# Optimization experiments

Hardware: AMD Instinct MI355X
Metric: run time of the kernel (lower is better)

The kernel has to match this reference:

```python
import jax, jax.numpy as jnp
import numpy as np

B, H, N, P = 2, 8, 2048, 64   # batch, heads, seq, head_dim
M, D = 4, 256                 # sketch count, sketch feature dim


def setup_inputs() -> dict:
    key = jax.random.key(0)
    kq, kk, ks, kr = jax.random.split(key, 4)
    scale = P ** -0.5  # keep exp(QK) numerically tame, std(dot) ~= 1/8
    Q = jax.random.normal(kq, (B, H, N, P), dtype=jnp.float32) * scale
    K = jax.random.normal(kk, (B, H, N, P), dtype=jnp.float32) * scale
    # indices into the concatenated [Q;K] token axis of length 2N
    sketching_matrix = jax.random.randint(ks, (B, M, D), 0, 2 * N)
    # Rademacher random signs, broadcast over [b,h,2n] in the reduction
    random_sign = jnp.sign(jax.random.normal(kr, (M, D), dtype=jnp.float32))
    random_sign = jnp.where(random_sign == 0, 1.0, random_sign)
    return {"Q": Q, "K": K, "sketching_matrix": sketching_matrix,
            "random_sign": random_sign}


def reference(Q, K, sketching_matrix, random_sign):
    b, h, n, p = Q.shape
    X = jnp.concatenate([Q, K], axis=2)          # [b,h,2n,p]
    Xt = jnp.transpose(X, (0, 2, 1, 3))          # [b,2n,h,p]
    # gather sketched landmarks: [b,m,d,h,p] -> [b,h,m,d,p]
    XS = Xt[jnp.arange(b)[:, None, None], sketching_matrix]
    XS = jnp.transpose(XS, (0, 3, 1, 2, 4))
    # RS_SM accumulate branch: exp of inner products, random-sign reduce over m
    product = jnp.einsum('bhnp,bhmdp->bhnmd', X, XS)   # [b,h,2n,m,d]
    AS = jnp.einsum('bhnmd,md->bhnd', jnp.exp(product), random_sign)
    return AS.astype(Q.dtype)                    # [b,h,2n,d]
```

## Files before the change

kernel.cpp:

```cpp
#include <hip/hip_runtime.h>
#include <hip/hip_bf16.h>

typedef __attribute__((ext_vector_type(8))) short short8;
typedef __attribute__((ext_vector_type(4))) float f32x4;

namespace {
constexpr int Nc  = 2048;
constexpr int NXc = 4096;
constexpr int Pc  = 64;
constexpr int Mc  = 4;
constexpr int Dc  = 256;
constexpr int BH  = 16;
constexpr int LDW = 72;
constexpr float LOG2E = 1.4426950408889634f;
}

__device__ inline float fexp2(float x) {
#if __has_builtin(__builtin_amdgcn_exp2f)
  return __builtin_amdgcn_exp2f(x);
#else
  return exp2f(x);
#endif
}

__device__ inline unsigned int bfpack(float a, float b) {
  union { __hip_bfloat162 h; unsigned int u; } cv;
  cv.h = __float22bfloat162_rn(make_float2(a, b));
  return cv.u;
}

__global__ __launch_bounds__(256) void prepass_kernel(
    const float* __restrict__ Q, const float* __restrict__ K,
    const int* __restrict__ SK,
    __hip_bfloat16* __restrict__ Xb, __hip_bfloat16* __restrict__ Wb)
{
  const int t = blockIdx.x * 256 + threadIdx.x;
  const int q = t & 7;
  const int r = t >> 3;
  const int NXROWS = BH * NXc;

  const float* src;
  __hip_bfloat16* dst;
  float scale;
  if (r < NXROWS) {
    const int bh = r >> 12, n = r & (NXc - 1);
    src = (n < Nc) ? (Q + ((size_t)bh * Nc + n) * Pc)
                   : (K + ((size_t)bh * Nc + (n - Nc)) * Pc);
    dst = Xb + (size_t)r * Pc;
    scale = 1.0f;
  } else {
    const int j  = r - NXROWS;
    const int bh = j >> 10;
    const int md = j & 1023;
    const int b  = bh >> 3;
    const int idx = SK[b * (Mc * Dc) + md];
    src = (idx < Nc) ? (Q + ((size_t)bh * Nc + idx) * Pc)
                     : (K + ((size_t)bh * Nc + (idx - Nc)) * Pc);
    dst = Wb + (size_t)j * Pc;
    scale = LOG2E;
  }
  const f32x4* s4 = (const f32x4*)(src + q * 8);
  f32x4 f0 = s4[0], f1 = s4[1];
  uint4 u;
  u.x = bfpack(f0.x * scale, f0.y * scale);
  u.y = bfpack(f0.z * scale, f0.w * scale);
  u.z = bfpack(f1.x * scale, f1.y * scale);
  u.w = bfpack(f1.z * scale, f1.w * scale);
  *(uint4*)(dst + q * 8) = u;
}

__global__ __launch_bounds__(256, 4) void sketch_main(
    const __hip_bfloat16* __restrict__ Xb, const __hip_bfloat16* __restrict__ Wb,
    const float* __restrict__ SGN, float* __restrict__ OUT)
{
  __shared__ __hip_bfloat16 Ws[2][64][LDW];
  __shared__ float Ss[Mc * Dc];

  const int t    = threadIdx.x;
  const int lane = t & 63;
  const int wv   = t >> 6;
  const int bh   = blockIdx.y;
  const int n0   = blockIdx.x * 64;

  for (int i = t; i < Mc * Dc; i += 256) Ss[i] = SGN[i];

  const int brow = lane & 15;
  const int acol = (lane >> 4) * 8;
  short8 afr[2];
  {
    const __hip_bfloat16* ap =
        Xb + ((size_t)bh * NXc + n0 + wv * 16 + brow) * Pc + acol;
    afr[0] = *(const short8*)ap;
    afr[1] = *(const short8*)(ap + 32);
  }

  const __hip_bfloat16* wbase = Wb + (size_t)bh * (Mc * Dc) * Pc;
  const int tr = t >> 2;
  const int tq = t & 3;

  auto crow = [](int p) { return (p & 3) * Dc + (p >> 2) * 64; };

  {
    const __hip_bfloat16* wp = wbase + (size_t)(crow(0) + tr) * Pc + tq * 16;
    uint4 wa = *(const uint4*)wp;
    uint4 wb = *(const uint4*)(wp + 8);
    *(uint4*)&Ws[0][tr][tq * 16]     = wa;
    *(uint4*)&Ws[0][tr][tq * 16 + 8] = wb;
  }
  __syncthreads();

  f32x4 AS[4];
  for (int tj = 0; tj < 4; ++tj) AS[tj] = (f32x4){0.f, 0.f, 0.f, 0.f};

  for (int p = 0; p < 16; ++p) {
    const int pn = (p < 15) ? p + 1 : 15;
    const __hip_bfloat16* wp = wbase + (size_t)(crow(pn) + tr) * Pc + tq * 16;
    uint4 wa = *(const uint4*)wp;
    uint4 wb = *(const uint4*)(wp + 8);

    const int buf = p & 1;
    short8 bfr[4][2];
    for (int tj = 0; tj < 4; ++tj) {
      bfr[tj][0] = *(const short8*)&Ws[buf][tj * 16 + brow][acol];
      bfr[tj][1] = *(const short8*)&Ws[buf][tj * 16 + brow][32 + acol];
    }
    const int m  = p & 3;
    const int dc = p >> 2;
    for (int tj = 0; tj < 4; ++tj) {
      f32x4 c = {0.f, 0.f, 0.f, 0.f};
      c = __builtin_amdgcn_mfma_f32_16x16x32_bf16(afr[0], bfr[tj][0], c, 0, 0, 0);
      c = __builtin_amdgcn_mfma_f32_16x16x32_bf16(afr[1], bfr[tj][1], c, 0, 0, 0);
      const float sg = Ss[m * Dc + dc * 64 + tj * 16 + brow];
      AS[tj].x = fmaf(sg, fexp2(c.x), AS[tj].x);
      AS[tj].y = fmaf(sg, fexp2(c.y), AS[tj].y);
      AS[tj].z = fmaf(sg, fexp2(c.z), AS[tj].z);
      AS[tj].w = fmaf(sg, fexp2(c.w), AS[tj].w);
    }

    if (m == 3) {
      const int nb    = n0 + wv * 16 + ((lane >> 4) << 2);
      const int dbase = dc * 64 + brow;
      for (int tj = 0; tj < 4; ++tj) {
        const size_t base = ((size_t)bh * NXc + nb) * Dc + dbase + tj * 16;
        OUT[base + 0 * (size_t)Dc] = AS[tj].x;
        OUT[base + 1 * (size_t)Dc] = AS[tj].y;
        OUT[base + 2 * (size_t)Dc] = AS[tj].z;
        OUT[base + 3 * (size_t)Dc] = AS[tj].w;
        AS[tj] = (f32x4){0.f, 0.f, 0.f, 0.f};
      }
    }

    *(uint4*)&Ws[buf ^ 1][tr][tq * 16]     = wa;
    *(uint4*)&Ws[buf ^ 1][tr][tq * 16 + 8] = wb;
    __syncthreads();
  }
}

extern "C" void kernel_launch(void* const* d_in, const int* in_sizes, int n_in,
                              void* d_out, int out_size, void* d_ws, size_t ws_size,
                              hipStream_t stream) {
  (void)in_sizes; (void)n_in; (void)out_size; (void)ws_size;
  const float* Q   = (const float*)d_in[0];
  const float* K   = (const float*)d_in[1];
  const int*   SK  = (const int*)d_in[2];
  const float* SGN = (const float*)d_in[3];
  float* OUT = (float*)d_out;

  __hip_bfloat16* Xb = (__hip_bfloat16*)d_ws;
  __hip_bfloat16* Wb = (__hip_bfloat16*)((char*)d_ws + (size_t)BH * NXc * Pc * 2);

  prepass_kernel<<<dim3(2560), dim3(256), 0, stream>>>(Q, K, SK, Xb, Wb);
  sketch_main<<<dim3(NXc / 64, BH), dim3(256), 0, stream>>>(Xb, Wb, SGN, OUT);
}
```

Baseline: 102.3 us.

## Swap MFMA operand roles, read landmarks from global, drop X prepass

The prepass now converts only the gathered landmark rows to bf16. The main kernel loads its Q/K rows directly as fp32 and converts them in registers. The MFMA operands are swapped so each lane holds 4 consecutive d outputs, which allows vectorized sign loads and contiguous float4 nontemporal stores. The shared-memory staging and per-step barriers for the landmarks are removed; each wave reads them straight from global/L2 instead. This raises register pressure (16 accumulators, launch bounds lowered to 3) and drops the double-buffered prefetch.

```diff
diff --git a/kernel.cpp b/kernel.cpp
--- a/kernel.cpp
+++ b/kernel.cpp
@@ -11,7 +11,6 @@
 constexpr int Mc  = 4;
 constexpr int Dc  = 256;
 constexpr int BH  = 16;
-constexpr int LDW = 72;
 constexpr float LOG2E = 1.4426950408889634f;
 }
 
@@ -31,129 +30,91 @@
 
 __global__ __launch_bounds__(256) void prepass_kernel(
     const float* __restrict__ Q, const float* __restrict__ K,
-    const int* __restrict__ SK,
-    __hip_bfloat16* __restrict__ Xb, __hip_bfloat16* __restrict__ Wb)
+    const int* __restrict__ SK, __hip_bfloat16* __restrict__ Wb)
 {
-  const int t = blockIdx.x * 256 + threadIdx.x;
-  const int q = t & 7;
-  const int r = t >> 3;
-  const int NXROWS = BH * NXc;
-
-  const float* src;
-  __hip_bfloat16* dst;
-  float scale;
-  if (r < NXROWS) {
-    const int bh = r >> 12, n = r & (NXc - 1);
-    src = (n < Nc) ? (Q + ((size_t)bh * Nc + n) * Pc)
-                   : (K + ((size_t)bh * Nc + (n - Nc)) * Pc);
-    dst = Xb + (size_t)r * Pc;
-    scale = 1.0f;
-  } else {
-    const int j  = r - NXROWS;
-    const int bh = j >> 10;
-    const int md = j & 1023;
-    const int b  = bh >> 3;
-    const int idx = SK[b * (Mc * Dc) + md];
-    src = (idx < Nc) ? (Q + ((size_t)bh * Nc + idx) * Pc)
-                     : (K + ((size_t)bh * Nc + (idx - Nc)) * Pc);
-    dst = Wb + (size_t)j * Pc;
-    scale = LOG2E;
-  }
+  const int t  = blockIdx.x * 256 + threadIdx.x;
+  const int q  = t & 7;
+  const int r  = t >> 3;
+  const int bh = r >> 10;
+  const int md = r & 1023;
+  const int b  = bh >> 3;
+  const int idx = SK[b * (Mc * Dc) + md];
+  const float* src = (idx < Nc) ? (Q + ((size_t)bh * Nc + idx) * Pc)
+                                : (K + ((size_t)bh * Nc + (idx - Nc)) * Pc);
   const f32x4* s4 = (const f32x4*)(src + q * 8);
   f32x4 f0 = s4[0], f1 = s4[1];
   uint4 u;
-  u.x = bfpack(f0.x * scale, f0.y * scale);
-  u.y = bfpack(f0.z * scale, f0.w * scale);
-  u.z = bfpack(f1.x * scale, f1.y * scale);
-  u.w = bfpack(f1.z * scale, f1.w * scale);
-  *(uint4*)(dst + q * 8) = u;
+  u.x = bfpack(f0.x * LOG2E, f0.y * LOG2E);
+  u.y = bfpack(f0.z * LOG2E, f0.w * LOG2E);
+  u.z = bfpack(f1.x * LOG2E, f1.y * LOG2E);
+  u.w = bfpack(f1.z * LOG2E, f1.w * LOG2E);
+  *(uint4*)(Wb + (size_t)r * Pc + q * 8) = u;
 }
 
-__global__ __launch_bounds__(256, 4) void sketch_main(
-    const __hip_bfloat16* __restrict__ Xb, const __hip_bfloat16* __restrict__ Wb,
+__global__ __launch_bounds__(256, 3) void sketch_main(
+    const float* __restrict__ Q, const float* __restrict__ K,
+    const __hip_bfloat16* __restrict__ Wb,
     const float* __restrict__ SGN, float* __restrict__ OUT)
 {
-  __shared__ __hip_bfloat16 Ws[2][64][LDW];
   __shared__ float Ss[Mc * Dc];
 
   const int t    = threadIdx.x;
   const int lane = t & 63;
   const int wv   = t >> 6;
+  const int brow = lane & 15;
+  const int q    = lane >> 4;
   const int bh   = blockIdx.y;
   const int n0   = blockIdx.x * 64;
 
   for (int i = t; i < Mc * Dc; i += 256) Ss[i] = SGN[i];
 
-  const int brow = lane & 15;
-  const int acol = (lane >> 4) * 8;
-  short8 afr[2];
+  const int nrow = n0 + wv * 16 + brow;
+  const float* xsrc = (n0 < Nc) ? (Q + ((size_t)bh * Nc + nrow) * Pc)
+                                : (K + ((size_t)bh * Nc + (nrow - Nc)) * Pc);
+  f32x4 x0 = *(const f32x4*)(xsrc + q * 8);
+  f32x4 x1 = *(const f32x4*)(xsrc + q * 8 + 4);
+  f32x4 x2 = *(const f32x4*)(xsrc + 32 + q * 8);
+  f32x4 x3 = *(const f32x4*)(xsrc + 32 + q * 8 + 4);
+  short8 bfr0, bfr1;
   {
-    const __hip_bfloat16* ap =
-        Xb + ((size_t)bh * NXc + n0 + wv * 16 + brow) * Pc + acol;
-    afr[0] = *(const short8*)ap;
-    afr[1] = *(const short8*)(ap + 32);
+    union { short8 s; uint4 u; } c0, c1;
+    c0.u.x = bfpack(x0.x, x0.y); c0.u.y = bfpack(x0.z, x0.w);
+    c0.u.z = bfpack(x1.x, x1.y); c0.u.w = bfpack(x1.z, x1.w);
+    c1.u.x = bfpack(x2.x, x2.y); c1.u.y = bfpack(x2.z, x2.w);
+    c1.u.z = bfpack(x3.x, x3.y); c1.u.w = bfpack(x3.z, x3.w);
+    bfr0 = c0.s; bfr1 = c1.s;
   }
 
-  const __hip_bfloat16* wbase = Wb + (size_t)bh * (Mc * Dc) * Pc;
-  const int tr = t >> 2;
-  const int tq = t & 3;
-
-  auto crow = [](int p) { return (p & 3) * Dc + (p >> 2) * 64; };
-
-  {
-    const __hip_bfloat16* wp = wbase + (size_t)(crow(0) + tr) * Pc + tq * 16;
-    uint4 wa = *(const uint4*)wp;
-    uint4 wb = *(const uint4*)(wp + 8);
-    *(uint4*)&Ws[0][tr][tq * 16]     = wa;
-    *(uint4*)&Ws[0][tr][tq * 16 + 8] = wb;
-  }
   __syncthreads();
 
-  f32x4 AS[4];
-  for (int tj = 0; tj < 4; ++tj) AS[tj] = (f32x4){0.f, 0.f, 0.f, 0.f};
+  const __hip_bfloat16* wb = Wb + (size_t)bh * (Mc * Dc) * Pc;
 
-  for (int p = 0; p < 16; ++p) {
-    const int pn = (p < 15) ? p + 1 : 15;
-    const __hip_bfloat16* wp = wbase + (size_t)(crow(pn) + tr) * Pc + tq * 16;
-    uint4 wa = *(const uint4*)wp;
-    uint4 wb = *(const uint4*)(wp + 8);
+  f32x4 AS[16];
+  #pragma unroll
+  for (int dt = 0; dt < 16; ++dt) AS[dt] = (f32x4){0.f, 0.f, 0.f, 0.f};
 
-    const int buf = p & 1;
-    short8 bfr[4][2];
-    for (int tj = 0; tj < 4; ++tj) {
-      bfr[tj][0] = *(const short8*)&Ws[buf][tj * 16 + brow][acol];
-      bfr[tj][1] = *(const short8*)&Ws[buf][tj * 16 + brow][32 + acol];
+  for (int m = 0; m < Mc; ++m) {
+    const __hip_bfloat16* wm = wb + (size_t)m * Dc * Pc;
+    #pragma unroll 4
+    for (int dt = 0; dt < 16; ++dt) {
+      const __hip_bfloat16* wrow = wm + (size_t)(dt * 16 + brow) * Pc + q * 8;
+      short8 a0 = *(const short8*)wrow;
+      short8 a1 = *(const short8*)(wrow + 32);
+      f32x4 c = {0.f, 0.f, 0.f, 0.f};
+      c = __builtin_amdgcn_mfma_f32_16x16x32_bf16(a0, bfr0, c, 0, 0, 0);
+      c = __builtin_amdgcn_mfma_f32_16x16x32_bf16(a1, bfr1, c, 0, 0, 0);
+      const f32x4 sg = *(const f32x4*)&Ss[m * Dc + dt * 16 + q * 4];
+      AS[dt].x = fmaf(sg.x, fexp2(c.x), AS[dt].x);
+      AS[dt].y = fmaf(sg.y, fexp2(c.y), AS[dt].y);
+      AS[dt].z = fmaf(sg.z, fexp2(c.z), AS[dt].z);
+      AS[dt].w = fmaf(sg.w, fexp2(c.w), AS[dt].w);
     }
-    const int m  = p & 3;
-    const int dc = p >> 2;
-    for (int tj = 0; tj < 4; ++tj) {
-      f32x4 c = {0.f, 0.f, 0.f, 0.f};
-      c = __builtin_amdgcn_mfma_f32_16x16x32_bf16(afr[0], bfr[tj][0], c, 0, 0, 0);
-      c = __builtin_amdgcn_mfma_f32_16x16x32_bf16(afr[1], bfr[tj][1], c, 0, 0, 0);
-      const float sg = Ss[m * Dc + dc * 64 + tj * 16 + brow];
-      AS[tj].x = fmaf(sg, fexp2(c.x), AS[tj].x);
-      AS[tj].y = fmaf(sg, fexp2(c.y), AS[tj].y);
-      AS[tj].z = fmaf(sg, fexp2(c.z), AS[tj].z);
-      AS[tj].w = fmaf(sg, fexp2(c.w), AS[tj].w);
-    }
+  }
 
-    if (m == 3) {
-      const int nb    = n0 + wv * 16 + ((lane >> 4) << 2);
-      const int dbase = dc * 64 + brow;
-      for (int tj = 0; tj < 4; ++tj) {
-        const size_t base = ((size_t)bh * NXc + nb) * Dc + dbase + tj * 16;
-        OUT[base + 0 * (size_t)Dc] = AS[tj].x;
-        OUT[base + 1 * (size_t)Dc] = AS[tj].y;
-        OUT[base + 2 * (size_t)Dc] = AS[tj].z;
-        OUT[base + 3 * (size_t)Dc] = AS[tj].w;
-        AS[tj] = (f32x4){0.f, 0.f, 0.f, 0.f};
-      }
-    }
-
-    *(uint4*)&Ws[buf ^ 1][tr][tq * 16]     = wa;
-    *(uint4*)&Ws[buf ^ 1][tr][tq * 16 + 8] = wb;
-    __syncthreads();
-  }
+  float* orow = OUT + ((size_t)bh * NXc + nrow) * Dc + q * 4;
+  #pragma unroll
+  for (int dt = 0; dt < 16; ++dt)
+    __builtin_nontemporal_store(AS[dt], (f32x4*)(orow + dt * 16));
 }
 
 extern "C" void kernel_launch(void* const* d_in, const int* in_sizes, int n_in,
@@ -166,9 +127,8 @@
   const float* SGN = (const float*)d_in[3];
   float* OUT = (float*)d_out;
 
-  __hip_bfloat16* Xb = (__hip_bfloat16*)d_ws;
-  __hip_bfloat16* Wb = (__hip_bfloat16*)((char*)d_ws + (size_t)BH * NXc * Pc * 2);
+  __hip_bfloat16* Wb = (__hip_bfloat16*)d_ws;
 
-  prepass_kernel<<<dim3(2560), dim3(256), 0, stream>>>(Q, K, SK, Xb, Wb);
-  sketch_main<<<dim3(NXc / 64, BH), dim3(256), 0, stream>>>(Xb, Wb, SGN, OUT);
+  prepass_kernel<<<dim3(512), dim3(256), 0, stream>>>(Q, K, SK, Wb);
+  sketch_main<<<dim3(NXc / 64, BH), dim3(256), 0, stream>>>(Q, K, Wb, SGN, OUT);
 }
```

Result: slower. 207.9 us (+103.2%).
